# Optimization experiments

Hardware: AMD Instinct MI355X
Metric: run time of the kernel (lower is better)

Reference implementation:

```python
import jax, jax.numpy as jnp
import numpy as np

B, S, D, H = 4, 2048, 1024, 16
HD = D // H


def setup_inputs() -> dict:
    key = jax.random.key(0)
    k1, k2, k3 = jax.random.split(key, 3)
    x = jax.random.normal(k1, (B, S, D), dtype=jnp.float32)
    # xavier-ish scaling for stable softmax
    W_attn = jax.random.normal(k2, (3 * D, D), dtype=jnp.float32) * (1.0 / np.sqrt(2 * D))
    b_attn = jnp.zeros((3 * D,), dtype=jnp.float32)
    W_out = jax.random.normal(k3, (D, D), dtype=jnp.float32) * (1.0 / np.sqrt(D))
    b_out = jnp.zeros((D,), dtype=jnp.float32)
    return {"x": x, "W_attn": W_attn, "b_attn": b_attn, "W_out": W_out, "b_out": b_out}


def reference(x, W_attn, b_attn, W_out, b_out):
    bs, seq, d = x.shape
    # fused QKV projection (torch Linear: y = x @ W.T + b)
    kqv = jnp.einsum("bsd,ed->bse", x, W_attn) + b_attn
    # NOTE: source splits as k, q, v (k first)
    k, q, v = jnp.split(kqv, 3, axis=2)
    # [b, s, h, hd] -> [b, h, s, hd]
    k = k.reshape(bs, seq, H, HD).transpose(0, 2, 1, 3)
    q = q.reshape(bs, seq, H, HD).transpose(0, 2, 1, 3)
    v = v.reshape(bs, seq, H, HD).transpose(0, 2, 1, 3)
    scale = 1.0 / np.sqrt(HD)
    scores = jnp.einsum("bhqd,bhkd->bhqk", q, k) * scale
    attn = jax.nn.softmax(scores, axis=-1)
    y = jnp.einsum("bhqk,bhkd->bhqd", attn, v)
    y = y.transpose(0, 2, 1, 3).reshape(bs, seq, d)
    out = jnp.einsum("bsd,ed->bse", y, W_out) + b_out
    return out
```

## Files before the change

### kernel.cpp

```cpp
#include <hip/hip_runtime.h>

typedef unsigned short u16;
typedef unsigned int u32;
typedef __attribute__((ext_vector_type(2))) u32 u32x2;
typedef __attribute__((ext_vector_type(4))) u32 u32x4;
typedef __attribute__((ext_vector_type(8))) short bf16x8;
typedef __attribute__((ext_vector_type(4))) float f32x4;

__device__ __forceinline__ u16 f2bf(float f) {
  u32 b = __float_as_uint(f);
  b += 0x7fffu + ((b >> 16) & 1u);
  return (u16)(b >> 16);
}

__device__ __forceinline__ u32 pk2bf(float a, float b) {
#if __has_builtin(__builtin_amdgcn_cvt_pk_bf16_f32)
  return __builtin_bit_cast(u32, __builtin_amdgcn_cvt_pk_bf16_f32(a, b));
#else
  return (u32)f2bf(a) | ((u32)f2bf(b) << 16);
#endif
}

__device__ __forceinline__ float fexp2(float x) {
#if __has_builtin(__builtin_amdgcn_exp2f)
  return __builtin_amdgcn_exp2f(x);
#else
  return exp2f(x);
#endif
}

__device__ __forceinline__ void gload_lds16(const u16* g, u16* l) {
  __builtin_amdgcn_global_load_lds((const __attribute__((address_space(1))) void*)g,
                                   (__attribute__((address_space(3))) void*)l, 16, 0, 0);
}

__global__ __launch_bounds__(256) void cvt_f32_bf16(const float* __restrict__ in,
                                                    u16* __restrict__ out) {
  long i = ((long)blockIdx.x * 256 + threadIdx.x) * 8;
  u32 u[8];
#pragma unroll
  for (int j = 0; j < 8; j++) {
    u32 b = __float_as_uint(in[i + j]);
    u[j] = (b + 0x7fffu + ((b >> 16) & 1u)) >> 16;
  }
  u32x4 o;
  o[0] = u[0] | (u[1] << 16);
  o[1] = u[2] | (u[3] << 16);
  o[2] = u[4] | (u[5] << 16);
  o[3] = u[6] | (u[7] << 16);
  *(u32x4*)(out + i) = o;
}

__device__ __forceinline__ void gemm_core_128(const u16* __restrict__ A,
                                              const u16* __restrict__ B, int K,
                                              int m0, int n0, u16* As, u16* Bs,
                                              f32x4 acc[4][4]) {
  int t = threadIdx.x;
  int lane = t & 63, w = t >> 6;
  int quad = lane >> 4, l16 = lane & 15;
  int wm = (w >> 1) * 64, wn = (w & 1) * 64;
  int lr = lane >> 3, lc = lane & 7;
  int cg = lc ^ lr;
  int swz = l16 & 7;
  for (int k0 = 0; k0 < K; k0 += 64) {
#pragma unroll
    for (int i = 0; i < 4; i++) {
      int r0 = i * 32 + w * 8;
      gload_lds16(&A[(long)(m0 + r0 + lr) * K + k0 + cg * 8], &As[r0 * 64]);
      gload_lds16(&B[(long)(n0 + r0 + lr) * K + k0 + cg * 8], &Bs[r0 * 64]);
    }
    __syncthreads();
#pragma unroll
    for (int ks = 0; ks < 2; ks++) {
      bf16x8 a[4], b[4];
#pragma unroll
      for (int tm = 0; tm < 4; tm++)
        a[tm] = *(const bf16x8*)&As[(wm + tm * 16 + l16) * 64 + ((ks * 4 + quad) ^ swz) * 8];
#pragma unroll
      for (int tn = 0; tn < 4; tn++)
        b[tn] = *(const bf16x8*)&Bs[(wn + tn * 16 + l16) * 64 + ((ks * 4 + quad) ^ swz) * 8];
#pragma unroll
      for (int tm = 0; tm < 4; tm++)
#pragma unroll
        for (int tn = 0; tn < 4; tn++)
          acc[tm][tn] = __builtin_amdgcn_mfma_f32_16x16x32_bf16(a[tm], b[tn],
                                                                acc[tm][tn], 0, 0, 0);
    }
    __syncthreads();
  }
}

#define QSCALE 0.1803368801f
__global__ __launch_bounds__(256) void gemm_qkv(const u16* __restrict__ W,
                                                const u16* __restrict__ X,
                                                const float* __restrict__ bias,
                                                u16* __restrict__ Kg,
                                                u16* __restrict__ Qg,
                                                u16* __restrict__ Vg) {
  __shared__ __align__(16) u16 As[128 * 64];
  __shared__ __align__(16) u16 Bs[128 * 64];
  const int K = 1024;
  int lin = blockIdx.x;
  int xcd = lin & 7, idx = lin >> 3;
  int mb = (idx % 12) + 12 * (xcd & 1);
  int sb = (idx / 12) + 16 * (xcd >> 1);
  int m0 = mb * 128, n0 = sb * 128;
  f32x4 acc[4][4];
#pragma unroll
  for (int i = 0; i < 4; i++)
#pragma unroll
    for (int j = 0; j < 4; j++) acc[i][j] = (f32x4)0.0f;
  gemm_core_128(W, X, K, m0, n0, As, Bs, acc);

  int t = threadIdx.x, lane = t & 63, w = t >> 6;
  int quad = lane >> 4, l16 = lane & 15;
  int wm = (w >> 1) * 64, wn = (w & 1) * 64;
  int which = m0 >> 10;
#pragma unroll
  for (int tm = 0; tm < 4; tm++) {
    int nf0 = m0 + wm + tm * 16 + quad * 4;
    int h = (nf0 >> 6) & 15, d0 = nf0 & 63;
    f32x4 bv = *(const f32x4*)&bias[nf0];
#pragma unroll
    for (int tn = 0; tn < 4; tn++) {
      int s_abs = n0 + wn + tn * 16 + l16;
      int b = s_abs >> 11, s = s_abs & 2047;
      long bh = (long)b * 16 + h;
      f32x4 v;
#pragma unroll
      for (int r = 0; r < 4; r++) v[r] = acc[tm][tn][r] + bv[r];
      if (which == 0) {
        u32x2 pk;
        pk[0] = pk2bf(v[0], v[1]);
        pk[1] = pk2bf(v[2], v[3]);
        *(u32x2*)&Kg[(bh * 2048 + s) * 64 + d0] = pk;
      } else if (which == 1) {
        u32x2 pk;
        pk[0] = pk2bf(v[0] * QSCALE, v[1] * QSCALE);
        pk[1] = pk2bf(v[2] * QSCALE, v[3] * QSCALE);
        *(u32x2*)&Qg[(bh * 2048 + s) * 64 + d0] = pk;
      } else {
#pragma unroll
        for (int r = 0; r < 4; r++)
          Vg[(bh * 64 + d0 + r) * 2048 + s] = f2bf(v[r]);
      }
    }
  }
}

__global__ __launch_bounds__(256) void gemm_out(const u16* __restrict__ W,
                                                const u16* __restrict__ Y,
                                                const float* __restrict__ bias,
                                                float* __restrict__ out) {
  __shared__ __align__(16) u16 As[128 * 64];
  __shared__ __align__(16) u16 Bs[128 * 64];
  const int K = 1024;
  int lin = blockIdx.x;
  int xcd = lin & 7, idx = lin >> 3;
  int mb = idx & 7;
  int sb = (idx >> 3) + 8 * xcd;
  int m0 = mb * 128, n0 = sb * 128;
  f32x4 acc[4][4];
#pragma unroll
  for (int i = 0; i < 4; i++)
#pragma unroll
    for (int j = 0; j < 4; j++) acc[i][j] = (f32x4)0.0f;
  gemm_core_128(W, Y, K, m0, n0, As, Bs, acc);

  int t = threadIdx.x, lane = t & 63, w = t >> 6;
  int quad = lane >> 4, l16 = lane & 15;
  int wm = (w >> 1) * 64, wn = (w & 1) * 64;
#pragma unroll
  for (int tm = 0; tm < 4; tm++) {
    int nf0 = m0 + wm + tm * 16 + quad * 4;
    f32x4 bv = *(const f32x4*)&bias[nf0];
#pragma unroll
    for (int tn = 0; tn < 4; tn++) {
      int s_abs = n0 + wn + tn * 16 + l16;
      f32x4 o;
#pragma unroll
      for (int r = 0; r < 4; r++) o[r] = acc[tm][tn][r] + bv[r];
      *(f32x4*)&out[(long)s_abs * 1024 + nf0] = o;
    }
  }
}

__global__ __launch_bounds__(256, 2) void attn_kernel(const u16* __restrict__ Qg,
                                                      const u16* __restrict__ Kg,
                                                      const u16* __restrict__ Vg,
                                                      u16* __restrict__ Y) {
  __shared__ __align__(16) u16 Ks[2][64 * 64];
  __shared__ __align__(16) u16 Vs[2][64 * 64];
  __shared__ __align__(16) u16 Ps[4 * 64 * 64];
  int t = threadIdx.x, lane = t & 63, w = t >> 6;
  int quad = lane >> 4, l16 = lane & 15;
  int lin = blockIdx.x;
  int bh = (lin & 7) + (lin >> 6) * 8;
  int qc = (lin >> 3) & 7;
  int q0 = qc * 256 + w * 64;
  u16* Pw = Ps + w * 64 * 64;
  int lr = lane >> 3, lc = lane & 7, cg = lc ^ lr;
  int swz = l16 & 7;

  const u16* Kbase = Kg + (long)bh * 2048 * 64;
  const u16* Vbase = Vg + (long)bh * 64 * 2048;

  bf16x8 qf[4][2];
#pragma unroll
  for (int tq = 0; tq < 4; tq++) {
    const u16* qp = Qg + ((long)bh * 2048 + q0 + tq * 16 + l16) * 64;
    qf[tq][0] = *(const bf16x8*)(qp + quad * 8);
    qf[tq][1] = *(const bf16x8*)(qp + 32 + quad * 8);
  }

  float lsum[4] = {0.0f, 0.0f, 0.0f, 0.0f};
  f32x4 acc[4][4];
#pragma unroll
  for (int tn = 0; tn < 4; tn++)
#pragma unroll
    for (int tq = 0; tq < 4; tq++) acc[tn][tq] = (f32x4)0.0f;

#pragma unroll
  for (int j = 0; j < 2; j++) {
    int r0 = j * 32 + w * 8;
    gload_lds16(&Kbase[(long)(r0 + lr) * 64 + cg * 8], &Ks[0][r0 * 64]);
    gload_lds16(&Vbase[(long)(r0 + lr) * 2048 + cg * 8], &Vs[0][r0 * 64]);
  }
  __syncthreads();

  for (int tile = 0; tile < 32; tile++) {
    const u16* Kc = Ks[tile & 1];
    const u16* Vc = Vs[tile & 1];
    if (tile + 1 < 32) {
      int kv0 = (tile + 1) * 64;
      u16* Kn = Ks[(tile + 1) & 1];
      u16* Vn = Vs[(tile + 1) & 1];
#pragma unroll
      for (int j = 0; j < 2; j++) {
        int r0 = j * 32 + w * 8;
        gload_lds16(&Kbase[(long)(kv0 + r0 + lr) * 64 + cg * 8], &Kn[r0 * 64]);
        gload_lds16(&Vbase[(long)(r0 + lr) * 2048 + kv0 + cg * 8], &Vn[r0 * 64]);
      }
    }

    bf16x8 kf[4][2];
#pragma unroll
    for (int tn = 0; tn < 4; tn++)
#pragma unroll
      for (int ks = 0; ks < 2; ks++)
        kf[tn][ks] = *(const bf16x8*)&Kc[(tn * 16 + l16) * 64 + ((ks * 4 + quad) ^ swz) * 8];

#pragma unroll
    for (int tq = 0; tq < 4; tq++) {
      f32x4 s[4];
#pragma unroll
      for (int tn = 0; tn < 4; tn++) s[tn] = (f32x4)0.0f;
#pragma unroll
      for (int ks = 0; ks < 2; ks++)
#pragma unroll
        for (int tn = 0; tn < 4; tn++)
          s[tn] = __builtin_amdgcn_mfma_f32_16x16x32_bf16(kf[tn][ks], qf[tq][ks],
                                                          s[tn], 0, 0, 0);
      int qrow = tq * 16 + l16;
#pragma unroll
      for (int tn = 0; tn < 4; tn++) {
        float e0 = fexp2(s[tn][0]);
        float e1 = fexp2(s[tn][1]);
        float e2 = fexp2(s[tn][2]);
        float e3 = fexp2(s[tn][3]);
        lsum[tq] += (e0 + e1) + (e2 + e3);
        u32x2 pk;
        pk[0] = pk2bf(e0, e1);
        pk[1] = pk2bf(e2, e3);
        int c2 = ((tn * 2 + (quad >> 1)) ^ swz) * 2 + (quad & 1);
        *(u32x2*)&Pw[qrow * 64 + c2 * 4] = pk;
      }
    }

#pragma unroll
    for (int ks = 0; ks < 2; ks++) {
      bf16x8 vf[4];
#pragma unroll
      for (int tn = 0; tn < 4; tn++)
        vf[tn] = *(const bf16x8*)&Vc[(tn * 16 + l16) * 64 + ((ks * 4 + quad) ^ swz) * 8];
#pragma unroll
      for (int tq = 0; tq < 4; tq++) {
        bf16x8 pf = *(const bf16x8*)&Pw[(tq * 16 + l16) * 64 + ((ks * 4 + quad) ^ swz) * 8];
#pragma unroll
        for (int tn = 0; tn < 4; tn++)
          acc[tn][tq] = __builtin_amdgcn_mfma_f32_16x16x32_bf16(vf[tn], pf,
                                                                acc[tn][tq], 0, 0, 0);
      }
    }
    __syncthreads();
  }

#pragma unroll
  for (int tq = 0; tq < 4; tq++) {
    lsum[tq] += __shfl_xor(lsum[tq], 16, 64);
    lsum[tq] += __shfl_xor(lsum[tq], 32, 64);
  }

  int b = bh >> 4, h = bh & 15;
#pragma unroll
  for (int tq = 0; tq < 4; tq++) {
    float inv = 1.0f / lsum[tq];
    long row = (long)b * 2048 + q0 + tq * 16 + l16;
#pragma unroll
    for (int tn = 0; tn < 4; tn++) {
      u32x2 pk;
      pk[0] = pk2bf(acc[tn][tq][0] * inv, acc[tn][tq][1] * inv);
      pk[1] = pk2bf(acc[tn][tq][2] * inv, acc[tn][tq][3] * inv);
      *(u32x2*)&Y[row * 1024 + h * 64 + tn * 16 + quad * 4] = pk;
    }
  }
}

extern "C" void kernel_launch(void* const* d_in, const int* in_sizes, int n_in,
                              void* d_out, int out_size, void* d_ws, size_t ws_size,
                              hipStream_t stream) {
  const float* x = (const float*)d_in[0];
  const float* W_attn = (const float*)d_in[1];
  const float* b_attn = (const float*)d_in[2];
  const float* W_out = (const float*)d_in[3];
  const float* b_out = (const float*)d_in[4];
  float* out = (float*)d_out;

  char* ws = (char*)d_ws;
  u16* xb = (u16*)ws;
  u16* Wab = (u16*)(ws + 16777216);
  u16* Wob = (u16*)(ws + 16777216 + 6291456);
  u16* Kg = (u16*)(ws + 25165824);
  u16* Qg = Kg + 8388608;
  u16* Vg = Qg + 8388608;
  u16* Yb = xb;

  cvt_f32_bf16<<<4096, 256, 0, stream>>>(x, xb);
  cvt_f32_bf16<<<1536, 256, 0, stream>>>(W_attn, Wab);
  cvt_f32_bf16<<<512, 256, 0, stream>>>(W_out, Wob);

  gemm_qkv<<<1536, 256, 0, stream>>>(Wab, xb, b_attn, Kg, Qg, Vg);
  attn_kernel<<<512, 256, 0, stream>>>(Qg, Kg, Vg, Yb);
  gemm_out<<<512, 256, 0, stream>>>(Wob, Yb, b_out, out);
}
```

Before: 289.6 us.

## Split attention KV range across wave pairs, load K/V directly to registers

The attention kernel now gives each block 128 query rows. The four waves form two pairs that each process half the key/value tiles (split-K), and the partial outputs and row sums are reduced through shared memory at the end. K/V tiles are loaded straight from global memory into registers with double buffering, replacing the LDS staging and the per-tile __syncthreads. The grid doubles to 1024 blocks. This should give more parallelism and remove barrier stalls, at the cost of twice as much global K/V traffic per query row, more register pressure, and an extra reduction pass.

```diff
diff --git a/kernel.cpp b/kernel.cpp
--- a/kernel.cpp
+++ b/kernel.cpp
@@ -185,21 +185,78 @@
   }
 }
 
+__device__ __forceinline__ void ld_kv(const u16* Kb, const u16* Vb, int kv0,
+                                      int l16, int quad,
+                                      bf16x8 kf[4][2], bf16x8 vf[4][2]) {
+#pragma unroll
+  for (int tn = 0; tn < 4; tn++) {
+    const u16* kp = Kb + (long)(kv0 + tn * 16 + l16) * 64 + quad * 8;
+    kf[tn][0] = *(const bf16x8*)kp;
+    kf[tn][1] = *(const bf16x8*)(kp + 32);
+    const u16* vp = Vb + (long)(tn * 16 + l16) * 2048 + kv0 + quad * 8;
+    vf[tn][0] = *(const bf16x8*)vp;
+    vf[tn][1] = *(const bf16x8*)(vp + 32);
+  }
+}
+
+__device__ __forceinline__ void tile_compute(const bf16x8 kf[4][2],
+                                             const bf16x8 vf[4][2],
+                                             const bf16x8 qf[4][2], u16* Pw,
+                                             int l16, int quad, int swz,
+                                             float lsum[4], f32x4 acc[4][4]) {
+#pragma unroll
+  for (int tq = 0; tq < 4; tq++) {
+    f32x4 s[4];
+#pragma unroll
+    for (int tn = 0; tn < 4; tn++) s[tn] = (f32x4)0.0f;
+#pragma unroll
+    for (int ks = 0; ks < 2; ks++)
+#pragma unroll
+      for (int tn = 0; tn < 4; tn++)
+        s[tn] = __builtin_amdgcn_mfma_f32_16x16x32_bf16(kf[tn][ks], qf[tq][ks],
+                                                        s[tn], 0, 0, 0);
+    int qrow = tq * 16 + l16;
+#pragma unroll
+    for (int tn = 0; tn < 4; tn++) {
+      float e0 = fexp2(s[tn][0]);
+      float e1 = fexp2(s[tn][1]);
+      float e2 = fexp2(s[tn][2]);
+      float e3 = fexp2(s[tn][3]);
+      lsum[tq] += (e0 + e1) + (e2 + e3);
+      u32x2 pk;
+      pk[0] = pk2bf(e0, e1);
+      pk[1] = pk2bf(e2, e3);
+      int c2 = ((tn * 2 + (quad >> 1)) ^ swz) * 2 + (quad & 1);
+      *(u32x2*)&Pw[qrow * 64 + c2 * 4] = pk;
+    }
+  }
+#pragma unroll
+  for (int ks = 0; ks < 2; ks++) {
+#pragma unroll
+    for (int tq = 0; tq < 4; tq++) {
+      bf16x8 pf = *(const bf16x8*)&Pw[(tq * 16 + l16) * 64 + ((ks * 4 + quad) ^ swz) * 8];
+#pragma unroll
+      for (int tn = 0; tn < 4; tn++)
+        acc[tn][tq] = __builtin_amdgcn_mfma_f32_16x16x32_bf16(vf[tn][ks], pf,
+                                                              acc[tn][tq], 0, 0, 0);
+    }
+  }
+}
+
 __global__ __launch_bounds__(256, 2) void attn_kernel(const u16* __restrict__ Qg,
                                                       const u16* __restrict__ Kg,
                                                       const u16* __restrict__ Vg,
                                                       u16* __restrict__ Y) {
-  __shared__ __align__(16) u16 Ks[2][64 * 64];
-  __shared__ __align__(16) u16 Vs[2][64 * 64];
   __shared__ __align__(16) u16 Ps[4 * 64 * 64];
+  __shared__ float Ls[2][64];
   int t = threadIdx.x, lane = t & 63, w = t >> 6;
+  int wq = w >> 1, wk = w & 1;
   int quad = lane >> 4, l16 = lane & 15;
   int lin = blockIdx.x;
-  int bh = (lin & 7) + (lin >> 6) * 8;
-  int qc = (lin >> 3) & 7;
-  int q0 = qc * 256 + w * 64;
+  int bh = (lin & 7) + (lin >> 7) * 8;
+  int qc = (lin >> 3) & 15;
+  int q0 = qc * 128 + wq * 64;
   u16* Pw = Ps + w * 64 * 64;
-  int lr = lane >> 3, lc = lane & 7, cg = lc ^ lr;
   int swz = l16 & 7;
 
   const u16* Kbase = Kg + (long)bh * 2048 * 64;
@@ -220,79 +277,15 @@
 #pragma unroll
     for (int tq = 0; tq < 4; tq++) acc[tn][tq] = (f32x4)0.0f;
 
-#pragma unroll
-  for (int j = 0; j < 2; j++) {
-    int r0 = j * 32 + w * 8;
-    gload_lds16(&Kbase[(long)(r0 + lr) * 64 + cg * 8], &Ks[0][r0 * 64]);
-    gload_lds16(&Vbase[(long)(r0 + lr) * 2048 + cg * 8], &Vs[0][r0 * 64]);
-  }
-  __syncthreads();
-
-  for (int tile = 0; tile < 32; tile++) {
-    const u16* Kc = Ks[tile & 1];
-    const u16* Vc = Vs[tile & 1];
-    if (tile + 1 < 32) {
-      int kv0 = (tile + 1) * 64;
-      u16* Kn = Ks[(tile + 1) & 1];
-      u16* Vn = Vs[(tile + 1) & 1];
-#pragma unroll
-      for (int j = 0; j < 2; j++) {
-        int r0 = j * 32 + w * 8;
-        gload_lds16(&Kbase[(long)(kv0 + r0 + lr) * 64 + cg * 8], &Kn[r0 * 64]);
-        gload_lds16(&Vbase[(long)(r0 + lr) * 2048 + kv0 + cg * 8], &Vn[r0 * 64]);
-      }
-    }
-
-    bf16x8 kf[4][2];
-#pragma unroll
-    for (int tn = 0; tn < 4; tn++)
-#pragma unroll
-      for (int ks = 0; ks < 2; ks++)
-        kf[tn][ks] = *(const bf16x8*)&Kc[(tn * 16 + l16) * 64 + ((ks * 4 + quad) ^ swz) * 8];
-
-#pragma unroll
-    for (int tq = 0; tq < 4; tq++) {
-      f32x4 s[4];
-#pragma unroll
-      for (int tn = 0; tn < 4; tn++) s[tn] = (f32x4)0.0f;
-#pragma unroll
-      for (int ks = 0; ks < 2; ks++)
-#pragma unroll
-        for (int tn = 0; tn < 4; tn++)
-          s[tn] = __builtin_amdgcn_mfma_f32_16x16x32_bf16(kf[tn][ks], qf[tq][ks],
-                                                          s[tn], 0, 0, 0);
-      int qrow = tq * 16 + l16;
-#pragma unroll
-      for (int tn = 0; tn < 4; tn++) {
-        float e0 = fexp2(s[tn][0]);
-        float e1 = fexp2(s[tn][1]);
-        float e2 = fexp2(s[tn][2]);
-        float e3 = fexp2(s[tn][3]);
-        lsum[tq] += (e0 + e1) + (e2 + e3);
-        u32x2 pk;
-        pk[0] = pk2bf(e0, e1);
-        pk[1] = pk2bf(e2, e3);
-        int c2 = ((tn * 2 + (quad >> 1)) ^ swz) * 2 + (quad & 1);
-        *(u32x2*)&Pw[qrow * 64 + c2 * 4] = pk;
-      }
-    }
-
-#pragma unroll
-    for (int ks = 0; ks < 2; ks++) {
-      bf16x8 vf[4];
-#pragma unroll
-      for (int tn = 0; tn < 4; tn++)
-        vf[tn] = *(const bf16x8*)&Vc[(tn * 16 + l16) * 64 + ((ks * 4 + quad) ^ swz) * 8];
-#pragma unroll
-      for (int tq = 0; tq < 4; tq++) {
-        bf16x8 pf = *(const bf16x8*)&Pw[(tq * 16 + l16) * 64 + ((ks * 4 + quad) ^ swz) * 8];
-#pragma unroll
-        for (int tn = 0; tn < 4; tn++)
-          acc[tn][tq] = __builtin_amdgcn_mfma_f32_16x16x32_bf16(vf[tn], pf,
-                                                                acc[tn][tq], 0, 0, 0);
-      }
-    }
-    __syncthreads();
+  bf16x8 kfa[4][2], vfa[4][2], kfb[4][2], vfb[4][2];
+  ld_kv(Kbase, Vbase, wk * 64, l16, quad, kfa, vfa);
+#pragma unroll 1
+  for (int i = 0; i < 16; i += 2) {
+    ld_kv(Kbase, Vbase, (i + 1) * 128 + wk * 64, l16, quad, kfb, vfb);
+    tile_compute(kfa, vfa, qf, Pw, l16, quad, swz, lsum, acc);
+    if (i + 2 < 16)
+      ld_kv(Kbase, Vbase, (i + 2) * 128 + wk * 64, l16, quad, kfa, vfa);
+    tile_compute(kfb, vfb, qf, Pw, l16, quad, swz, lsum, acc);
   }
 
 #pragma unroll
@@ -301,17 +294,43 @@
     lsum[tq] += __shfl_xor(lsum[tq], 32, 64);
   }
 
-  int b = bh >> 4, h = bh & 15;
-#pragma unroll
-  for (int tq = 0; tq < 4; tq++) {
-    float inv = 1.0f / lsum[tq];
-    long row = (long)b * 2048 + q0 + tq * 16 + l16;
-#pragma unroll
-    for (int tn = 0; tn < 4; tn++) {
-      u32x2 pk;
-      pk[0] = pk2bf(acc[tn][tq][0] * inv, acc[tn][tq][1] * inv);
-      pk[1] = pk2bf(acc[tn][tq][2] * inv, acc[tn][tq][3] * inv);
-      *(u32x2*)&Y[row * 1024 + h * 64 + tn * 16 + quad * 4] = pk;
+  __syncthreads();
+
+  if (wk == 1) {
+    float* fb = (float*)Ps + (w >> 1) * 4096;
+#pragma unroll
+    for (int tn = 0; tn < 4; tn++)
+#pragma unroll
+      for (int tq = 0; tq < 4; tq++)
+        *(f32x4*)&fb[(tq * 16 + l16) * 64 + ((tn * 4 + quad) ^ l16) * 4] = acc[tn][tq];
+    if (quad == 0)
+#pragma unroll
+      for (int tq = 0; tq < 4; tq++) Ls[wq][tq * 16 + l16] = lsum[tq];
+  }
+  __syncthreads();
+
+  if (wk == 0) {
+    const float* fb = (const float*)Ps + (w >> 1) * 4096;
+#pragma unroll
+    for (int tn = 0; tn < 4; tn++)
+#pragma unroll
+      for (int tq = 0; tq < 4; tq++) {
+        f32x4 p = *(const f32x4*)&fb[(tq * 16 + l16) * 64 + ((tn * 4 + quad) ^ l16) * 4];
+#pragma unroll
+        for (int r = 0; r < 4; r++) acc[tn][tq][r] += p[r];
+      }
+    int b = bh >> 4, h = bh & 15;
+#pragma unroll
+    for (int tq = 0; tq < 4; tq++) {
+      float inv = 1.0f / (lsum[tq] + Ls[wq][tq * 16 + l16]);
+      long row = (long)b * 2048 + q0 + tq * 16 + l16;
+#pragma unroll
+      for (int tn = 0; tn < 4; tn++) {
+        u32x2 pk;
+        pk[0] = pk2bf(acc[tn][tq][0] * inv, acc[tn][tq][1] * inv);
+        pk[1] = pk2bf(acc[tn][tq][2] * inv, acc[tn][tq][3] * inv);
+        *(u32x2*)&Y[row * 1024 + h * 64 + tn * 16 + quad * 4] = pk;
+      }
     }
   }
 }
@@ -340,6 +359,6 @@
   cvt_f32_bf16<<<512, 256, 0, stream>>>(W_out, Wob);
 
   gemm_qkv<<<1536, 256, 0, stream>>>(Wab, xb, b_attn, Kg, Qg, Vg);
-  attn_kernel<<<512, 256, 0, stream>>>(Qg, Kg, Vg, Yb);
+  attn_kernel<<<1024, 256, 0, stream>>>(Qg, Kg, Vg, Yb);
   gemm_out<<<512, 256, 0, stream>>>(Wob, Yb, b_out, out);
 }
```

New measurement: 427.8 us. +47.7%, slower.
